# Kernel optimization log

Measured on AMD Instinct MI355X. Metric: run time of the kernel, lower is better.

Reference implementation:

```python
import jax, jax.numpy as jnp
import numpy as np

# ---- constants mirroring the torch module ----
OSAMP = 8            # temporal oversampling factor
MAX_ITER = 10        # forward solver iterations (LBFGS replaced by fixed GD)
NEG_SHIFT = 2 * OSAMP
OTP = 5              # baseline frames subtracted from ctc/aif
C_SHARP = 500.0      # sharpness constant C=500 in fermi_ir_func
LR = 0.1             # fixed step size for the deterministic forward solve


def interp_linear_1d(x, size):
    # interp_linear_1D: linear upsampling along last (time) axis
    return jax.image.resize(x, x.shape[:-1] + (size,), method='linear')


def fermi_ir(eta, t_os):
    # eta: [B,3,H,W] = (amplitude A, decay rate k, delay t0); t_os: [Tos]
    tsh = t_os - t_os[NEG_SHIFT]                    # negative time shift
    A = eta[:, 0][..., None]                        # [B,H,W,1]
    k = eta[:, 1][..., None]
    t0 = eta[:, 2][..., None]
    step = jax.nn.sigmoid(C_SHARP * tsh)            # sharp causal onset (C=500)
    return A * jax.nn.sigmoid(k * (t0 - tsh)) * step  # [B,H,W,Tos]


def convolve(aif, ir):
    # linear convolution along time via FFT; output aligned with neg_shift offset
    Tos = ir.shape[-1]
    n = 2 * Tos
    Fa = jnp.fft.rfft(aif, n=n, axis=-1)            # [B,1,1,n/2+1]
    Fi = jnp.fft.rfft(ir, n=n, axis=-1)             # [B,H,W,n/2+1]
    full = jnp.fft.irfft(Fa * Fi, n=n, axis=-1)
    return jax.lax.dynamic_slice_in_dim(full, NEG_SHIFT, Tos, axis=-1)


def make_objective(ctc, aif, time, eta_prior, lambda_reg):
    # preprocessing from FermiDataConsLBFGS.forward
    aif = aif - aif[..., :OTP].mean(-1, keepdims=True)
    ctc = ctc - ctc[..., :OTP].mean(-1, keepdims=True)
    Tos = OSAMP * ctc.shape[-1]
    aif_os = interp_linear_1d(aif, Tos)
    ctc_os = interp_linear_1d(ctc, Tos)
    t_os = interp_linear_1d(time, Tos)
    ctc_dc = ctc_os[..., ::OSAMP]                   # [B,H,W,T]
    C_nn = (eta_prior ** 2).sum(axis=(0, 2, 3), keepdims=True)  # [1,3,1,1]
    C_dc = (ctc_dc ** 2).sum()
    sp_lam = jax.nn.softplus(lambda_reg).squeeze()

    def F_obj(eta):  # FermiDConsObj.__call__ (OD disabled: indx_dc = all frames)
        ir = fermi_ir(eta, t_os)
        ctc_est = convolve(aif_os, ir)[..., ::OSAMP] / OSAMP
        dc = ((ctc_dc - ctc_est) ** 2 / C_dc).sum()
        reg = sp_lam * (((eta - eta_prior) ** 2) / C_nn).sum()
        pos = (jax.nn.relu(-eta) ** 2).sum()
        return dc + reg + pos
    return F_obj


def setup_inputs():
    key = jax.random.key(0)
    k1, k2, k3, k4 = jax.random.split(key, 4)
    B, H, W, T = 1, 128, 128, 64
    ctc = jax.random.normal(k1, (B, H, W, T), jnp.float32) * 0.1
    aif = jax.random.uniform(k2, (B, 1, 1, T), jnp.float32)
    time = jnp.arange(T, dtype=jnp.float32)
    seg = jnp.ones((B, H, W), jnp.int32)
    eta_nn = jax.random.uniform(k3, (B, 3, H, W), jnp.float32)
    lambda_reg = jax.random.normal(k4, (1,), jnp.float32)
    return {"ctc": ctc, "aif": aif, "time": time, "seg": seg,
            "eta_nn": eta_nn, "lambda_reg": lambda_reg}


def reference(ctc, aif, time, seg, eta_nn, lambda_reg):
    # seg only affects the (disabled) outlier-detection path
    F_obj = make_objective(ctc, aif, time, eta_nn, lambda_reg)
    gradF = jax.grad(F_obj)

    def step(eta, _):
        return eta - LR * gradF(eta), None

    eta_pi, _ = jax.lax.scan(step, eta_nn, None, length=MAX_ITER)
    return eta_pi
```

## Files before the change

### kernel.cpp

```cpp
#include <hip/hip_runtime.h>
#include <math.h>

#define T_IN 64
#define NPIX 16384
#define MAX_ITER 10
#define NSLOT 43
#define MAGIC 0x13579BDFu

typedef _Float16 half8_t __attribute__((ext_vector_type(8)));
typedef __fp16   fp16x2  __attribute__((ext_vector_type(2)));
typedef float    f32x4   __attribute__((ext_vector_type(4)));
typedef int      i32x4   __attribute__((ext_vector_type(4)));

union H8 { half8_t v; fp16x2 h2[4]; i32x4 i4; };

__device__ __forceinline__ float rcp_fast(float x) { return __builtin_amdgcn_rcpf(x); }

__constant__ constexpr int NTMIN[16] = {0,0,0,0,0,1,1,1,1,2,2,2,2,3,3,3};
__constant__ constexpr int TOFS[16]  = {0,4,8,12,16,20,23,26,29,32,34,36,38,40,41,42};

template<int KT>
__device__ __forceinline__ void buildTile(float T0, float nK, float r, int q,
        const float (&d10b)[16], const float (&tse0)[8], const float (&tse15)[8],
        H8& F0h, H8& F1h, H8& F2h) {
    float  x[8];
    fp16x2 d1h[4];
    float  d10 = T0 - d10b[KT];
    const fp16x2 c1 = {(__fp16)0.25f, (__fp16)0.25f};
    const fp16x2 c2 = {(__fp16)0.50f, (__fp16)0.50f};
    const fp16x2 c3 = {(__fp16)0.75f, (__fp16)0.75f};
    bool arith = true;
    if constexpr (KT == 0 || KT == 15) {
        bool flat = (KT == 0) ? (q == 0) : (q == 3);
        if (flat) {
            arith = false;
            const float* te;
            if constexpr (KT == 0) te = tse0; else te = tse15;
            #pragma unroll
            for (int j = 0; j < 8; ++j) x[j] = __expf(nK * (T0 - te[j]));
            #pragma unroll
            for (int jj = 0; jj < 4; ++jj)
                d1h[jj] = __builtin_amdgcn_cvt_pkrtz(T0 - te[2*jj],
                                                     T0 - te[2*jj+1]);
        }
    }
    if (arith) {
        x[0] = __expf(nK * d10);
        x[4] = __expf(nK * (d10 - 0.5f));
        x[1] = x[0]*r; x[2] = x[1]*r; x[3] = x[2]*r;
        x[5] = x[4]*r; x[6] = x[5]*r; x[7] = x[6]*r;
        fp16x2 D0 = __builtin_amdgcn_cvt_pkrtz(d10, d10 - 0.125f);
        d1h[0] = D0;
        d1h[1] = D0 - c1;
        d1h[2] = D0 - c2;
        d1h[3] = D0 - c3;
    }
    #pragma unroll
    for (int jj = 0; jj < 4; ++jj) {
        float s1a = rcp_fast(1.0f + x[2*jj]);
        float s1b = rcp_fast(1.0f + x[2*jj+1]);
        fp16x2 sh = __builtin_amdgcn_cvt_pkrtz(s1a, s1b);
        fp16x2 eh = sh - sh*sh;
        F0h.h2[jj] = sh;
        F1h.h2[jj] = eh * d1h[jj];
        F2h.h2[jj] = eh;
    }
}

template<int KT>
struct Pipe {
    static __device__ __forceinline__ void run(float T0, float nK, float r, int q,
            const float (&d10b)[16], const float (&tse0)[8], const float (&tse15)[8],
            const i32x4 (&Breg)[NSLOT],
            H8 (&F0p)[2], H8 (&F1p)[2], H8 (&F2p)[2],
            f32x4 (&acc)[3][4]) {
        if constexpr (KT < 15)
            buildTile<KT+1>(T0, nK, r, q, d10b, tse0, tse15,
                            F0p[(KT+1)&1], F1p[(KT+1)&1], F2p[(KT+1)&1]);
        const f32x4 Z = (f32x4){0.f, 0.f, 0.f, 0.f};
        #pragma unroll
        for (int nt = NTMIN[KT]; nt < 4; ++nt) {
            int slot = TOFS[KT] + nt - NTMIN[KT];
            H8 bh; bh.i4 = Breg[slot];
            if constexpr (KT == 0) {
                acc[0][nt] = __builtin_amdgcn_mfma_f32_16x16x32_f16(F0p[0].v, bh.v, Z, 0, 0, 0);
                acc[1][nt] = __builtin_amdgcn_mfma_f32_16x16x32_f16(F1p[0].v, bh.v, Z, 0, 0, 0);
                acc[2][nt] = __builtin_amdgcn_mfma_f32_16x16x32_f16(F2p[0].v, bh.v, Z, 0, 0, 0);
            } else {
                acc[0][nt] = __builtin_amdgcn_mfma_f32_16x16x32_f16(F0p[KT&1].v, bh.v, acc[0][nt], 0, 0, 0);
                acc[1][nt] = __builtin_amdgcn_mfma_f32_16x16x32_f16(F1p[KT&1].v, bh.v, acc[1][nt], 0, 0, 0);
                acc[2][nt] = __builtin_amdgcn_mfma_f32_16x16x32_f16(F2p[KT&1].v, bh.v, acc[2][nt], 0, 0, 0);
            }
        }
        if constexpr (KT < 15)
            Pipe<KT+1>::run(T0, nK, r, q, d10b, tse0, tse15, Breg, F0p, F1p, F2p, acc);
    }
};

__global__ __launch_bounds__(256, 1) void k_all(
        const float* __restrict__ ctc,  const float* __restrict__ aif,
        const float* __restrict__ timev,const float* __restrict__ lam,
        const float* __restrict__ eta,  unsigned int* __restrict__ flags,
        f32x4* __restrict__ partials,   float* __restrict__ out) {
    __shared__ i32x4 Bs[NSLOT * 64];
    __shared__ float tshs[512];
    __shared__ float aifos[512];
    __shared__ float a_s[64], t_s[64];
    __shared__ f32x4 red[4];

    const int tid  = threadIdx.x;
    const int lane = tid & 63;
    const int wid  = tid >> 6;
    const int q = lane >> 4, n = lane & 15;
    const int pixbase = blockIdx.x * 64 + wid * 16;
    const int mypix   = pixbase + n;

    if (tid < 64) { a_s[tid] = aif[tid]; t_s[tid] = timev[tid]; }
    float A  = eta[mypix];
    float K  = eta[NPIX + mypix];
    float T0 = eta[2*NPIX + mypix];
    const float pA = A, pK = K, pT = T0;
    __syncthreads();
    {
        float m5a = 0.2f * (a_s[0]+a_s[1]+a_s[2]+a_s[3]+a_s[4]);
        float t16;
        {
            float xx = 1.5625f; int i0 = (int)xx; float f = xx - (float)i0;
            t16 = t_s[i0]*(1.0f-f) + t_s[i0+1]*f;
        }
        #pragma unroll
        for (int rep = 0; rep < 2; ++rep) {
            int i = tid + 256*rep;
            float x = ((float)i - 3.5f) * 0.125f;
            float ao, to;
            if (x <= 0.0f)       { ao = a_s[0]  - m5a; to = t_s[0];  }
            else if (x >= 63.0f) { ao = a_s[63] - m5a; to = t_s[63]; }
            else {
                int i0 = (int)x; float f = x - (float)i0;
                ao = (a_s[i0]-m5a)*(1.0f-f) + (a_s[i0+1]-m5a)*f;
                to = t_s[i0]*(1.0f-f) + t_s[i0+1]*f;
            }
            aifos[i] = ao;
            tshs[i]  = to - t16;
        }
    }

    float dcreg[4][4];
    #pragma unroll
    for (int reg = 0; reg < 4; ++reg) {
        const float* cp = ctc + (pixbase + q*4 + reg) * T_IN;
        float m5 = 0.2f * (cp[0]+cp[1]+cp[2]+cp[3]+cp[4]);
        #pragma unroll
        for (int nt = 0; nt < 4; ++nt) {
            int d = nt*16 + n;
            float cc = cp[d] - m5;
            float cm = cp[(d > 0) ? d-1 : 0] - m5;
            dcreg[nt][reg] = (d == 0) ? cc : (0.4375f*cm + 0.5625f*cc);
        }
    }

    {
        float vs = 0.f;
        #pragma unroll
        for (int nt = 0; nt < 4; ++nt)
            #pragma unroll
            for (int r2 = 0; r2 < 4; ++r2) vs += dcreg[nt][r2]*dcreg[nt][r2];
        f32x4 pv = (f32x4){vs, 0.25f*A*A, 0.25f*K*K, 0.25f*T0*T0};
        #pragma unroll
        for (int m = 1; m < 64; m <<= 1) {
            pv.x += __shfl_xor(pv.x, m); pv.y += __shfl_xor(pv.y, m);
            pv.z += __shfl_xor(pv.z, m); pv.w += __shfl_xor(pv.w, m);
        }
        if (lane == 0) red[wid] = pv;
    }
    __syncthreads();
    if (tid == 0) {
        f32x4 s = red[0] + red[1] + red[2] + red[3];
        partials[blockIdx.x] = s;
        __threadfence();
        __hip_atomic_store(&flags[blockIdx.x], MAGIC, __ATOMIC_RELEASE,
                           __HIP_MEMORY_SCOPE_AGENT);
    }

    for (int idx = tid; idx < NSLOT * 64; idx += 256) {
        int slot = idx >> 6, l = idx & 63;
        int kt, nt;
        if (slot < 20)      { kt = slot >> 2; nt = slot & 3; }
        else if (slot < 32) { int s = slot - 20; int d3 = s / 3; kt = 5 + d3; nt = 1 + (s - 3*d3); }
        else if (slot < 40) { int s = slot - 32; kt = 9 + (s >> 1); nt = 2 + (s & 1); }
        else                { kt = 13 + (slot - 40); nt = 3; }
        int kbase = 32*kt + 8*(l >> 4);
        int m = 16 + 8 * (16*nt + (l & 15));
        H8 bh;
        #pragma unroll
        for (int jj = 0; jj < 4; ++jj) {
            float v[2];
            #pragma unroll
            for (int h = 0; h < 2; ++h) {
                int k  = kbase + 2*jj + h;
                int ai = m - k;
                float s2 = 1.0f / (1.0f + __expf(-500.0f * tshs[k]));
                v[h] = (ai >= 0 && ai < 512) ? s2 * aifos[ai] * 0.125f : 0.0f;
            }
            bh.h2[jj] = (fp16x2){(__fp16)v[0], (__fp16)v[1]};
        }
        Bs[idx] = bh.i4;
    }
    __syncthreads();

    i32x4 Breg[NSLOT];
    #pragma unroll
    for (int s = 0; s < NSLOT; ++s) Breg[s] = Bs[s*64 + lane];

    float  d10b[16];
    float  tse0[8], tse15[8];
    #pragma unroll
    for (int kt = 0; kt < 16; ++kt) d10b[kt] = tshs[32*kt + 8*q];
    #pragma unroll
    for (int j = 0; j < 8; ++j) { tse0[j] = tshs[8*q + j]; tse15[j] = tshs[480 + 8*q + j]; }

    while (__hip_atomic_load(&flags[tid], __ATOMIC_ACQUIRE,
                             __HIP_MEMORY_SCOPE_AGENT) != MAGIC)
        __builtin_amdgcn_s_sleep(2);
    __syncthreads();

    f32x4 tot = partials[lane] + partials[64+lane] + partials[128+lane]
              + partials[192+lane];
    #pragma unroll
    for (int m = 1; m < 64; m <<= 1) {
        tot.x += __shfl_xor(tot.x, m); tot.y += __shfl_xor(tot.y, m);
        tot.z += __shfl_xor(tot.z, m); tot.w += __shfl_xor(tot.w, m);
    }
    float spl;
    {
        float xl = lam[0];
        spl = (xl > 0.0f) ? (xl + log1pf(__expf(-xl))) : log1pf(__expf(xl));
    }
    const float cdc2 = 2.0f / tot.x;
    const float rgA  = 2.0f * spl / tot.y;
    const float rgK  = 2.0f * spl / tot.z;
    const float rgT  = 2.0f * spl / tot.w;

    #pragma unroll 1
    for (int it = 0; it < MAX_ITER; ++it) {
        float nK = -K;
        float r  = __expf(0.125f * K);

        H8 F0p[2], F1p[2], F2p[2];
        f32x4 acc[3][4];
        buildTile<0>(T0, nK, r, q, d10b, tse0, tse15, F0p[0], F1p[0], F2p[0]);
        Pipe<0>::run(T0, nK, r, q, d10b, tse0, tse15, Breg, F0p, F1p, F2p, acc);

        float Ap[4];
        #pragma unroll
        for (int rr2 = 0; rr2 < 4; ++rr2) Ap[rr2] = __shfl(A, q*4 + rr2);

        float SA[4], SK[4], ST[4];
        #pragma unroll
        for (int r2 = 0; r2 < 4; ++r2) { SA[r2]=0.f; SK[r2]=0.f; ST[r2]=0.f; }
        #pragma unroll
        for (int nt = 0; nt < 4; ++nt)
            #pragma unroll
            for (int r2 = 0; r2 < 4; ++r2) {
                float Y0 = acc[0][nt][r2], Y1 = acc[1][nt][r2], Y2 = acc[2][nt][r2];
                float rr = fmaf(Ap[r2], Y0, -dcreg[nt][r2]);
                SA[r2] = fmaf(rr, Y0, SA[r2]);
                SK[r2] = fmaf(rr, Y1, SK[r2]);
                ST[r2] = fmaf(rr, Y2, ST[r2]);
            }
        #pragma unroll
        for (int r2 = 0; r2 < 4; ++r2)
            #pragma unroll
            for (int m = 1; m < 16; m <<= 1) {
                SA[r2] += __shfl_xor(SA[r2], m);
                SK[r2] += __shfl_xor(SK[r2], m);
                ST[r2] += __shfl_xor(ST[r2], m);
            }
        int src = (n >> 2) * 16;
        float GA = 0.f, GK = 0.f, GT = 0.f;
        #pragma unroll
        for (int r2 = 0; r2 < 4; ++r2) {
            float tA = __shfl(SA[r2], src);
            float tK = __shfl(SK[r2], src);
            float tT = __shfl(ST[r2], src);
            if ((n & 3) == r2) { GA = tA; GK = tK; GT = tT; }
        }

        float gA = fmaf(rgA, A  - pA, cdc2 * GA)         + 2.0f * fminf(A,  0.f);
        float gK = fmaf(rgK, K  - pK, cdc2 * A * GK)     + 2.0f * fminf(K,  0.f);
        float gT = fmaf(rgT, T0 - pT, cdc2 * A * K * GT) + 2.0f * fminf(T0, 0.f);
        A  -= 0.1f * gA;
        K  -= 0.1f * gK;
        T0 -= 0.1f * gT;
    }

    if (lane < 16) {
        out[mypix]          = A;
        out[NPIX + mypix]   = K;
        out[2*NPIX + mypix] = T0;
    }
}

extern "C" void kernel_launch(void* const* d_in, const int* in_sizes, int n_in,
                              void* d_out, int out_size, void* d_ws, size_t ws_size,
                              hipStream_t stream) {
    const float* ctc   = (const float*)d_in[0];
    const float* aif   = (const float*)d_in[1];
    const float* timev = (const float*)d_in[2];
    const float* eta   = (const float*)d_in[4];
    const float* lam   = (const float*)d_in[5];
    float* out = (float*)d_out;
    f32x4*        partials = (f32x4*)d_ws;
    unsigned int* flags    = (unsigned int*)((char*)d_ws + 4096);

    k_all<<<NPIX / 64, 256, 0, stream>>>(ctc, aif, timev, lam, eta,
                                         flags, partials, out);
}
```

Baseline: 114.2 us.

## Split K-dimension MFMA pipeline across wave pairs with LDS partial-sum exchange

```diff
diff --git a/kernel.cpp b/kernel.cpp
--- a/kernel.cpp
+++ b/kernel.cpp
@@ -68,36 +68,100 @@
 }
 
 template<int KT>
-struct Pipe {
-    static __device__ __forceinline__ void run(float T0, float nK, float r, int q,
+struct Pipe2 {
+    static __device__ __forceinline__ void run(float T0, float nK, float r, int q, int lane,
             const float (&d10b)[16], const float (&tse0)[8], const float (&tse15)[8],
-            const i32x4 (&Breg)[NSLOT],
+            const i32x4* __restrict__ Bs,
             H8 (&F0p)[2], H8 (&F1p)[2], H8 (&F2p)[2],
             f32x4 (&acc)[3][4]) {
-        if constexpr (KT < 15)
-            buildTile<KT+1>(T0, nK, r, q, d10b, tse0, tse15,
-                            F0p[(KT+1)&1], F1p[(KT+1)&1], F2p[(KT+1)&1]);
+        constexpr int PB = (KT >> 1) & 1;
+        if constexpr (KT + 2 < 16)
+            buildTile<KT+2>(T0, nK, r, q, d10b, tse0, tse15,
+                            F0p[PB^1], F1p[PB^1], F2p[PB^1]);
         const f32x4 Z = (f32x4){0.f, 0.f, 0.f, 0.f};
         #pragma unroll
         for (int nt = NTMIN[KT]; nt < 4; ++nt) {
             int slot = TOFS[KT] + nt - NTMIN[KT];
-            H8 bh; bh.i4 = Breg[slot];
-            if constexpr (KT == 0) {
-                acc[0][nt] = __builtin_amdgcn_mfma_f32_16x16x32_f16(F0p[0].v, bh.v, Z, 0, 0, 0);
-                acc[1][nt] = __builtin_amdgcn_mfma_f32_16x16x32_f16(F1p[0].v, bh.v, Z, 0, 0, 0);
-                acc[2][nt] = __builtin_amdgcn_mfma_f32_16x16x32_f16(F2p[0].v, bh.v, Z, 0, 0, 0);
+            H8 bh; bh.i4 = Bs[slot*64 + lane];
+            if constexpr (KT < 2) {
+                acc[0][nt] = __builtin_amdgcn_mfma_f32_16x16x32_f16(F0p[PB].v, bh.v, Z, 0, 0, 0);
+                acc[1][nt] = __builtin_amdgcn_mfma_f32_16x16x32_f16(F1p[PB].v, bh.v, Z, 0, 0, 0);
+                acc[2][nt] = __builtin_amdgcn_mfma_f32_16x16x32_f16(F2p[PB].v, bh.v, Z, 0, 0, 0);
             } else {
-                acc[0][nt] = __builtin_amdgcn_mfma_f32_16x16x32_f16(F0p[KT&1].v, bh.v, acc[0][nt], 0, 0, 0);
-                acc[1][nt] = __builtin_amdgcn_mfma_f32_16x16x32_f16(F1p[KT&1].v, bh.v, acc[1][nt], 0, 0, 0);
-                acc[2][nt] = __builtin_amdgcn_mfma_f32_16x16x32_f16(F2p[KT&1].v, bh.v, acc[2][nt], 0, 0, 0);
+                acc[0][nt] = __builtin_amdgcn_mfma_f32_16x16x32_f16(F0p[PB].v, bh.v, acc[0][nt], 0, 0, 0);
+                acc[1][nt] = __builtin_amdgcn_mfma_f32_16x16x32_f16(F1p[PB].v, bh.v, acc[1][nt], 0, 0, 0);
+                acc[2][nt] = __builtin_amdgcn_mfma_f32_16x16x32_f16(F2p[PB].v, bh.v, acc[2][nt], 0, 0, 0);
             }
         }
-        if constexpr (KT < 15)
-            Pipe<KT+1>::run(T0, nK, r, q, d10b, tse0, tse15, Breg, F0p, F1p, F2p, acc);
+        if constexpr (KT + 2 < 16)
+            Pipe2<KT+2>::run(T0, nK, r, q, lane, d10b, tse0, tse15, Bs, F0p, F1p, F2p, acc);
     }
 };
 
-__global__ __launch_bounds__(256, 1) void k_all(
+template<int H>
+__device__ __forceinline__ void pipeAcc(float T0, float nK, float r, int q, int lane,
+        const float (&d10b)[16], const float (&tse0)[8], const float (&tse15)[8],
+        const i32x4* __restrict__ Bs, f32x4 (&acc)[3][4]) {
+    H8 F0p[2], F1p[2], F2p[2];
+    buildTile<H>(T0, nK, r, q, d10b, tse0, tse15, F0p[0], F1p[0], F2p[0]);
+    Pipe2<H>::run(T0, nK, r, q, lane, d10b, tse0, tse15, Bs, F0p, F1p, F2p, acc);
+}
+
+template<int H>
+__device__ __forceinline__ void sendHalf(const f32x4 (&acc)[3][4],
+        float2* __restrict__ xch, int pair, int lane) {
+    constexpr int SB = 2 - 2*H;
+    float2* xw = xch + ((pair*2 + H)*12)*64 + lane;
+    #pragma unroll
+    for (int i = 0; i < 3; ++i)
+        #pragma unroll
+        for (int nt = 0; nt < 4; ++nt)
+            xw[(i*4+nt)*64] = make_float2(acc[i][nt][SB], acc[i][nt][SB+1]);
+}
+
+template<int H>
+__device__ __forceinline__ void finishDots(f32x4 (&acc)[3][4],
+        const float2* __restrict__ xch, float (&Gtab)[4][16][4],
+        int pair, int lane, int q, int n,
+        const float (&dcreg)[4][4], float A) {
+    constexpr int KB = 2*H;
+    const float2* xr = xch + ((pair*2 + (1-H))*12)*64 + lane;
+    #pragma unroll
+    for (int i = 0; i < 3; ++i)
+        #pragma unroll
+        for (int nt = 0; nt < 4; ++nt) {
+            float2 v = xr[(i*4+nt)*64];
+            acc[i][nt][KB]   += v.x;
+            acc[i][nt][KB+1] += v.y;
+        }
+    float Ap0 = __shfl(A, q*4 + KB);
+    float Ap1 = __shfl(A, q*4 + KB + 1);
+    float SA0=0.f,SK0=0.f,ST0=0.f, SA1=0.f,SK1=0.f,ST1=0.f;
+    #pragma unroll
+    for (int nt = 0; nt < 4; ++nt) {
+        float Y0 = acc[0][nt][KB], Y1 = acc[1][nt][KB], Y2 = acc[2][nt][KB];
+        float rr = fmaf(Ap0, Y0, -dcreg[nt][KB]);
+        SA0 = fmaf(rr, Y0, SA0); SK0 = fmaf(rr, Y1, SK0); ST0 = fmaf(rr, Y2, ST0);
+        float y0 = acc[0][nt][KB+1], y1 = acc[1][nt][KB+1], y2 = acc[2][nt][KB+1];
+        float r2 = fmaf(Ap1, y0, -dcreg[nt][KB+1]);
+        SA1 = fmaf(r2, y0, SA1); SK1 = fmaf(r2, y1, SK1); ST1 = fmaf(r2, y2, ST1);
+    }
+    #pragma unroll
+    for (int m = 1; m < 16; m <<= 1) {
+        SA0 += __shfl_xor(SA0, m); SK0 += __shfl_xor(SK0, m); ST0 += __shfl_xor(ST0, m);
+        SA1 += __shfl_xor(SA1, m); SK1 += __shfl_xor(SK1, m); ST1 += __shfl_xor(ST1, m);
+    }
+    if (n == 0) {
+        float* g = Gtab[pair][q*4 + KB];
+        g[0] = SA0; g[1] = SK0; g[2] = ST0;
+    }
+    if (n == 1) {
+        float* g = Gtab[pair][q*4 + KB + 1];
+        g[0] = SA1; g[1] = SK1; g[2] = ST1;
+    }
+}
+
+__global__ __launch_bounds__(512, 2) void k_all(
         const float* __restrict__ ctc,  const float* __restrict__ aif,
         const float* __restrict__ timev,const float* __restrict__ lam,
         const float* __restrict__ eta,  unsigned int* __restrict__ flags,
@@ -106,13 +170,17 @@
     __shared__ float tshs[512];
     __shared__ float aifos[512];
     __shared__ float a_s[64], t_s[64];
-    __shared__ f32x4 red[4];
+    __shared__ f32x4 red[8];
+    __shared__ float2 xch[2*4*12*64];
+    __shared__ float Gtab[4][16][4];
 
     const int tid  = threadIdx.x;
     const int lane = tid & 63;
     const int wid  = tid >> 6;
+    const int hh   = wid & 1;
+    const int pair = wid >> 1;
     const int q = lane >> 4, n = lane & 15;
-    const int pixbase = blockIdx.x * 64 + wid * 16;
+    const int pixbase = blockIdx.x * 64 + pair * 16;
     const int mypix   = pixbase + n;
 
     if (tid < 64) { a_s[tid] = aif[tid]; t_s[tid] = timev[tid]; }
@@ -128,21 +196,18 @@
             float xx = 1.5625f; int i0 = (int)xx; float f = xx - (float)i0;
             t16 = t_s[i0]*(1.0f-f) + t_s[i0+1]*f;
         }
-        #pragma unroll
-        for (int rep = 0; rep < 2; ++rep) {
-            int i = tid + 256*rep;
-            float x = ((float)i - 3.5f) * 0.125f;
-            float ao, to;
-            if (x <= 0.0f)       { ao = a_s[0]  - m5a; to = t_s[0];  }
-            else if (x >= 63.0f) { ao = a_s[63] - m5a; to = t_s[63]; }
-            else {
-                int i0 = (int)x; float f = x - (float)i0;
-                ao = (a_s[i0]-m5a)*(1.0f-f) + (a_s[i0+1]-m5a)*f;
-                to = t_s[i0]*(1.0f-f) + t_s[i0+1]*f;
-            }
-            aifos[i] = ao;
-            tshs[i]  = to - t16;
-        }
+        int i = tid;
+        float x = ((float)i - 3.5f) * 0.125f;
+        float ao, to;
+        if (x <= 0.0f)       { ao = a_s[0]  - m5a; to = t_s[0];  }
+        else if (x >= 63.0f) { ao = a_s[63] - m5a; to = t_s[63]; }
+        else {
+            int i0 = (int)x; float f = x - (float)i0;
+            ao = (a_s[i0]-m5a)*(1.0f-f) + (a_s[i0+1]-m5a)*f;
+            to = t_s[i0]*(1.0f-f) + t_s[i0+1]*f;
+        }
+        aifos[i] = ao;
+        tshs[i]  = to - t16;
     }
 
     float dcreg[4][4];
@@ -165,7 +230,7 @@
         for (int nt = 0; nt < 4; ++nt)
             #pragma unroll
             for (int r2 = 0; r2 < 4; ++r2) vs += dcreg[nt][r2]*dcreg[nt][r2];
-        f32x4 pv = (f32x4){vs, 0.25f*A*A, 0.25f*K*K, 0.25f*T0*T0};
+        f32x4 pv = (f32x4){hh ? 0.f : vs, 0.125f*A*A, 0.125f*K*K, 0.125f*T0*T0};
         #pragma unroll
         for (int m = 1; m < 64; m <<= 1) {
             pv.x += __shfl_xor(pv.x, m); pv.y += __shfl_xor(pv.y, m);
@@ -175,14 +240,15 @@
     }
     __syncthreads();
     if (tid == 0) {
-        f32x4 s = red[0] + red[1] + red[2] + red[3];
+        f32x4 s = red[0] + red[1] + red[2] + red[3]
+                + red[4] + red[5] + red[6] + red[7];
         partials[blockIdx.x] = s;
         __threadfence();
         __hip_atomic_store(&flags[blockIdx.x], MAGIC, __ATOMIC_RELEASE,
                            __HIP_MEMORY_SCOPE_AGENT);
     }
 
-    for (int idx = tid; idx < NSLOT * 64; idx += 256) {
+    for (int idx = tid; idx < NSLOT * 64; idx += 512) {
         int slot = idx >> 6, l = idx & 63;
         int kt, nt;
         if (slot < 20)      { kt = slot >> 2; nt = slot & 3; }
@@ -208,10 +274,6 @@
     }
     __syncthreads();
 
-    i32x4 Breg[NSLOT];
-    #pragma unroll
-    for (int s = 0; s < NSLOT; ++s) Breg[s] = Bs[s*64 + lane];
-
     float  d10b[16];
     float  tse0[8], tse15[8];
     #pragma unroll
@@ -219,9 +281,11 @@
     #pragma unroll
     for (int j = 0; j < 8; ++j) { tse0[j] = tshs[8*q + j]; tse15[j] = tshs[480 + 8*q + j]; }
 
-    while (__hip_atomic_load(&flags[tid], __ATOMIC_ACQUIRE,
-                             __HIP_MEMORY_SCOPE_AGENT) != MAGIC)
-        __builtin_amdgcn_s_sleep(2);
+    if (tid < 256) {
+        while (__hip_atomic_load(&flags[tid], __ATOMIC_ACQUIRE,
+                                 __HIP_MEMORY_SCOPE_AGENT) != MAGIC)
+            __builtin_amdgcn_s_sleep(2);
+    }
     __syncthreads();
 
     f32x4 tot = partials[lane] + partials[64+lane] + partials[128+lane]
@@ -246,46 +310,22 @@
         float nK = -K;
         float r  = __expf(0.125f * K);
 
-        H8 F0p[2], F1p[2], F2p[2];
         f32x4 acc[3][4];
-        buildTile<0>(T0, nK, r, q, d10b, tse0, tse15, F0p[0], F1p[0], F2p[0]);
-        Pipe<0>::run(T0, nK, r, q, d10b, tse0, tse15, Breg, F0p, F1p, F2p, acc);
-
-        float Ap[4];
-        #pragma unroll
-        for (int rr2 = 0; rr2 < 4; ++rr2) Ap[rr2] = __shfl(A, q*4 + rr2);
-
-        float SA[4], SK[4], ST[4];
-        #pragma unroll
-        for (int r2 = 0; r2 < 4; ++r2) { SA[r2]=0.f; SK[r2]=0.f; ST[r2]=0.f; }
-        #pragma unroll
-        for (int nt = 0; nt < 4; ++nt)
-            #pragma unroll
-            for (int r2 = 0; r2 < 4; ++r2) {
-                float Y0 = acc[0][nt][r2], Y1 = acc[1][nt][r2], Y2 = acc[2][nt][r2];
-                float rr = fmaf(Ap[r2], Y0, -dcreg[nt][r2]);
-                SA[r2] = fmaf(rr, Y0, SA[r2]);
-                SK[r2] = fmaf(rr, Y1, SK[r2]);
-                ST[r2] = fmaf(rr, Y2, ST[r2]);
-            }
-        #pragma unroll
-        for (int r2 = 0; r2 < 4; ++r2)
-            #pragma unroll
-            for (int m = 1; m < 16; m <<= 1) {
-                SA[r2] += __shfl_xor(SA[r2], m);
-                SK[r2] += __shfl_xor(SK[r2], m);
-                ST[r2] += __shfl_xor(ST[r2], m);
-            }
-        int src = (n >> 2) * 16;
-        float GA = 0.f, GK = 0.f, GT = 0.f;
-        #pragma unroll
-        for (int r2 = 0; r2 < 4; ++r2) {
-            float tA = __shfl(SA[r2], src);
-            float tK = __shfl(SK[r2], src);
-            float tT = __shfl(ST[r2], src);
-            if ((n & 3) == r2) { GA = tA; GK = tK; GT = tT; }
-        }
-
+        if (hh == 0) {
+            pipeAcc<0>(T0, nK, r, q, lane, d10b, tse0, tse15, Bs, acc);
+            sendHalf<0>(acc, xch, pair, lane);
+        } else {
+            pipeAcc<1>(T0, nK, r, q, lane, d10b, tse0, tse15, Bs, acc);
+            sendHalf<1>(acc, xch, pair, lane);
+        }
+        __syncthreads();
+        if (hh == 0) finishDots<0>(acc, xch, Gtab, pair, lane, q, n, dcreg, A);
+        else         finishDots<1>(acc, xch, Gtab, pair, lane, q, n, dcreg, A);
+        __syncthreads();
+
+        const float GA = Gtab[pair][n][0];
+        const float GK = Gtab[pair][n][1];
+        const float GT = Gtab[pair][n][2];
         float gA = fmaf(rgA, A  - pA, cdc2 * GA)         + 2.0f * fminf(A,  0.f);
         float gK = fmaf(rgK, K  - pK, cdc2 * A * GK)     + 2.0f * fminf(K,  0.f);
         float gT = fmaf(rgT, T0 - pT, cdc2 * A * K * GT) + 2.0f * fminf(T0, 0.f);
@@ -294,7 +334,7 @@
         T0 -= 0.1f * gT;
     }
 
-    if (lane < 16) {
+    if (hh == 0 && lane < 16) {
         out[mypix]          = A;
         out[NPIX + mypix]   = K;
         out[2*NPIX + mypix] = T0;
@@ -313,6 +353,6 @@
     f32x4*        partials = (f32x4*)d_ws;
     unsigned int* flags    = (unsigned int*)((char*)d_ws + 4096);
 
-    k_all<<<NPIX / 64, 256, 0, stream>>>(ctc, aif, timev, lam, eta,
+    k_all<<<NPIX / 64, 512, 0, stream>>>(ctc, aif, timev, lam, eta,
                                          flags, partials, out);
 }
```

Result: slower. 117.1 us (+2.6%).
